# Kernel tuning notes

Hardware: AMD Instinct MI355X
Metric: run time of the kernel (lower is better)

The kernel has to match this reference:

```python
import jax, jax.numpy as jnp
import numpy as np

MEM_DIM = 4000
FEATURES = 2048
THRESHOLD = 1.0 / MEM_DIM
EPS = 1e-12
COS_EPS = 1e-8  # torch CosineSimilarity default eps


def setup_inputs() -> dict:
    key = jax.random.key(0)
    k1, k2 = jax.random.split(key)
    x = jax.random.normal(k1, (8192, FEATURES), dtype=jnp.float32)
    # kaiming_uniform_ with a=0: bound = sqrt(6 / fan_in), fan_in = FEATURES
    bound = float(np.sqrt(6.0 / FEATURES))
    memory = jax.random.uniform(k2, (MEM_DIM, FEATURES), dtype=jnp.float32,
                                minval=-bound, maxval=bound)
    return {"x": x, "memory": memory}


def reference(x, memory):
    # Cosine similarity via normalized matmul: [b, MEM_DIM]
    z_norm = jnp.linalg.norm(x, axis=1)              # [b]
    m_norm = jnp.linalg.norm(memory, axis=1)         # [M]
    logits = (x @ memory.T) / jnp.maximum(z_norm[:, None] * m_norm[None, :], COS_EPS)
    w = jax.nn.softmax(logits, axis=1)               # [b, M]
    # sparse shrinkage: relu(w - t) * w / (|w - t| + eps)
    d = w - THRESHOLD
    w = jnp.maximum(d, 0.0) * w / (jnp.abs(d) + EPS)
    # L1 normalize over memory dim (F.normalize p=1, eps=1e-12)
    w = w / jnp.maximum(jnp.sum(jnp.abs(w), axis=1, keepdims=True), EPS)
    return w @ memory                                # [b, features]
```

## Files before the change

kernel.cpp:

```cpp
#include <hip/hip_runtime.h>
#include <hip/hip_fp16.h>
#include <math.h>

#define FEATURES 2048
#define MROWS 4000
#define NPAD 4096
#define BROWS 8192

typedef unsigned short u16;
typedef unsigned int u32;

typedef __attribute__((ext_vector_type(8))) _Float16 f16x8;
typedef __attribute__((ext_vector_type(8))) short s16x8;
typedef __attribute__((ext_vector_type(4))) float f32x4;

__device__ __forceinline__ u16 f2h(float f) {
  union { _Float16 h; u16 u; } cv;
  cv.h = (_Float16)f;
  return cv.u;
}
__device__ __forceinline__ u16 f2bf(float f) {
  u32 u = __float_as_uint(f);
  u32 r = (u + 0x7FFFu + ((u >> 16) & 1u)) >> 16;
  return (u16)r;
}
__device__ __forceinline__ float bf2f(u16 h) {
  return __uint_as_float(((u32)h) << 16);
}

#define GLD16(g, l)                                                            \
  __builtin_amdgcn_global_load_lds(                                            \
      (const __attribute__((address_space(1))) u32*)(g),                       \
      (__attribute__((address_space(3))) u32*)(l), 16, 0, 0)

__global__ __launch_bounds__(256) void conv_split_bf16_kernel(
    const float* __restrict__ src, u16* __restrict__ hi, u16* __restrict__ lo,
    float* __restrict__ norms, int nrows) {
  __shared__ float red[4];
  const int row = blockIdx.x;
  const int tid = threadIdx.x;
  ushort4* hp = (ushort4*)(hi + (size_t)row * FEATURES);
  ushort4* lp = (ushort4*)(lo + (size_t)row * FEATURES);
  float ss = 0.f;
  if (row < nrows) {
    const float4* sp = (const float4*)(src + (size_t)row * FEATURES);
#pragma unroll
    for (int p = 0; p < 2; ++p) {
      const int idx = tid + p * 256;
      float4 f = sp[idx];
      ushort4 h, l;
      h.x = f2bf(f.x); l.x = f2bf(f.x - bf2f(h.x)); ss += f.x * f.x;
      h.y = f2bf(f.y); l.y = f2bf(f.y - bf2f(h.y)); ss += f.y * f.y;
      h.z = f2bf(f.z); l.z = f2bf(f.z - bf2f(h.z)); ss += f.z * f.z;
      h.w = f2bf(f.w); l.w = f2bf(f.w - bf2f(h.w)); ss += f.w * f.w;
      hp[idx] = h;
      lp[idx] = l;
    }
  } else {
    const ushort4 zz = {0, 0, 0, 0};
#pragma unroll
    for (int p = 0; p < 2; ++p) {
      hp[tid + p * 256] = zz;
      lp[tid + p * 256] = zz;
    }
  }
#pragma unroll
  for (int o = 32; o; o >>= 1) ss += __shfl_xor(ss, o);
  if ((tid & 63) == 0) red[tid >> 6] = ss;
  __syncthreads();
  if (tid == 0) {
    float tot = red[0] + red[1] + red[2] + red[3];
    norms[row] = (row < nrows) ? sqrtf(tot) : 1.0f;
  }
}

__global__ __launch_bounds__(256) void transpose_f16_kernel(
    const float* __restrict__ mem, u16* __restrict__ mt) {
  __shared__ float tile[64][65];
  const int tid = threadIdx.x;
  const int ti = blockIdx.x;
  const int tj = blockIdx.y;
  const int c = tid & 63;
  const int r0 = tid >> 6;
#pragma unroll
  for (int i = 0; i < 16; ++i) {
    const int r = i * 4 + r0;
    const int gr = ti * 64 + r;
    float v = 0.f;
    if (gr < MROWS) v = mem[(size_t)gr * FEATURES + tj * 64 + c];
    tile[r][c] = v;
  }
  __syncthreads();
#pragma unroll
  for (int i = 0; i < 16; ++i) {
    const int r = i * 4 + r0;
    mt[(size_t)(tj * 64 + r) * NPAD + ti * 64 + c] = f2h(tile[c][r]);
  }
}

__global__ __launch_bounds__(512, 2) void gemm1_kernel(
    const u16* __restrict__ Ah, const u16* __restrict__ Al,
    const u16* __restrict__ Bh, const u16* __restrict__ Bl,
    const float* __restrict__ zn, const float* __restrict__ mn,
    float* __restrict__ C) {
  __shared__ __align__(16) u16 sAh[2 * 8192];
  __shared__ __align__(16) u16 sAl[2 * 8192];
  __shared__ __align__(16) u16 sBh[2 * 8192];
  __shared__ __align__(16) u16 sBl[2 * 8192];
  const int tid = threadIdx.x;
  const int wid = tid >> 6;
  const int lane = tid & 63;
  const int brow = blockIdx.x * 256;
  const int bcol = blockIdx.y * 256;
  const int wr = wid >> 2;
  const int wc = wid & 3;
  const int fr = lane & 15, fq = lane >> 4;
  const int fqa = (fq ^ ((fr >> 1) & 3)) * 8;

  f32x4 acc[8][4];
#pragma unroll
  for (int m = 0; m < 8; ++m)
#pragma unroll
    for (int n = 0; n < 4; ++n) acc[m][n] = (f32x4){0.f, 0.f, 0.f, 0.f};

  const int r_st = tid >> 2;
  const int c_sw = (((tid & 3) ^ ((tid >> 3) & 3)) << 3);

#define STAGE1(cur, k0)                                                        \
  {                                                                            \
    _Pragma("unroll") for (int p = 0; p < 2; ++p) {                            \
      const int r = r_st + p * 128;                                            \
      const size_t offA = (size_t)(brow + r) * FEATURES + ((k0) + c_sw);       \
      const size_t offB = (size_t)(bcol + r) * FEATURES + ((k0) + c_sw);       \
      const int ldso = (cur) * 8192 + p * 4096 + wid * 512;                    \
      GLD16(Ah + offA, sAh + ldso);                                            \
      GLD16(Al + offA, sAl + ldso);                                            \
      GLD16(Bh + offB, sBh + ldso);                                            \
      GLD16(Bl + offB, sBl + ldso);                                            \
    }                                                                          \
  }

#define G1_COMPUTE(cur)                                                        \
  {                                                                            \
    const int bo = (cur) * 8192;                                               \
    s16x8 bh[4], bl[4];                                                        \
    _Pragma("unroll") for (int n = 0; n < 4; ++n) {                            \
      const int ro = bo + (wc * 64 + n * 16 + fr) * 32 + fqa;                  \
      bh[n] = *(const s16x8*)(sBh + ro);                                       \
      bl[n] = *(const s16x8*)(sBl + ro);                                       \
    }                                                                          \
    _Pragma("unroll") for (int m = 0; m < 8; ++m) {                            \
      const int ro = bo + (wr * 128 + m * 16 + fr) * 32 + fqa;                 \
      const s16x8 ah = *(const s16x8*)(sAh + ro);                              \
      const s16x8 al = *(const s16x8*)(sAl + ro);                              \
      _Pragma("unroll") for (int n = 0; n < 4; ++n) {                          \
        acc[m][n] = __builtin_amdgcn_mfma_f32_16x16x32_bf16(                   \
            ah, bh[n], acc[m][n], 0, 0, 0);                                    \
        acc[m][n] = __builtin_amdgcn_mfma_f32_16x16x32_bf16(                   \
            al, bh[n], acc[m][n], 0, 0, 0);                                    \
        acc[m][n] = __builtin_amdgcn_mfma_f32_16x16x32_bf16(                   \
            ah, bl[n], acc[m][n], 0, 0, 0);                                    \
      }                                                                        \
    }                                                                          \
  }

  STAGE1(0, 0);
  __syncthreads();
  for (int kt = 0; kt < 64; ++kt) {
    const int cur = kt & 1;
    if (kt < 63) STAGE1(cur ^ 1, (kt + 1) * 32);
    G1_COMPUTE(cur);
    __syncthreads();
  }
#undef STAGE1
#undef G1_COMPUTE

#pragma unroll
  for (int m = 0; m < 8; ++m) {
#pragma unroll
    for (int r = 0; r < 4; ++r) {
      const int row = brow + wr * 128 + m * 16 + fq * 4 + r;
      const float z = zn[row];
#pragma unroll
      for (int n = 0; n < 4; ++n) {
        const int col = bcol + wc * 64 + n * 16 + fr;
        const float denom = fmaxf(z * mn[col], 1e-8f);
        C[(size_t)row * NPAD + col] = acc[m][n][r] / denom;
      }
    }
  }
}

__global__ __launch_bounds__(256) void softmax_kernel(float* __restrict__ logits) {
  __shared__ float red[4];
  const int row = blockIdx.x;
  const int tid = threadIdx.x;
  const float* lp = logits + (size_t)row * NPAD;
  u16* W = (u16*)logits + (size_t)row * (2 * NPAD);
  float v[16];
  float lmax = -3.4e38f;
#pragma unroll
  for (int i = 0; i < 16; ++i) {
    const int c = tid + i * 256;
    v[i] = (c < MROWS) ? lp[c] : -3.4e38f;
    lmax = fmaxf(lmax, v[i]);
  }
#pragma unroll
  for (int o = 32; o; o >>= 1) lmax = fmaxf(lmax, __shfl_xor(lmax, o));
  if ((tid & 63) == 0) red[tid >> 6] = lmax;
  __syncthreads();
  lmax = fmaxf(fmaxf(red[0], red[1]), fmaxf(red[2], red[3]));

  float s = 0.f;
#pragma unroll
  for (int i = 0; i < 16; ++i) {
    const int c = tid + i * 256;
    if (c < MROWS) {
      v[i] = expf(v[i] - lmax);
      s += v[i];
    } else {
      v[i] = 0.f;
    }
  }
#pragma unroll
  for (int o = 32; o; o >>= 1) s += __shfl_xor(s, o);
  __syncthreads();
  if ((tid & 63) == 0) red[tid >> 6] = s;
  __syncthreads();
  const float Z = red[0] + red[1] + red[2] + red[3];

  const float THR = (float)(1.0 / 4000.0);
  float s2 = 0.f;
#pragma unroll
  for (int i = 0; i < 16; ++i) {
    float w = v[i] / Z;
    const float d = w - THR;
    w = fmaxf(d, 0.f) * w / (fabsf(d) + 1e-12f);
    v[i] = w;
    s2 += w;
  }
#pragma unroll
  for (int o = 32; o; o >>= 1) s2 += __shfl_xor(s2, o);
  __syncthreads();
  if ((tid & 63) == 0) red[tid >> 6] = s2;
  __syncthreads();
  const float S = fmaxf(red[0] + red[1] + red[2] + red[3], 1e-12f);

#pragma unroll
  for (int i = 0; i < 16; ++i) {
    const int c = tid + i * 256;
    W[c] = f2h(v[i] / S);
  }
}

__global__ __launch_bounds__(256) void gemm2_kernel(
    const u16* __restrict__ A, const u16* __restrict__ B,
    float* __restrict__ C) {
  __shared__ __align__(16) u16 sA[2 * 4096];
  __shared__ __align__(16) u16 sB[2 * 4096];
  const int tid = threadIdx.x;
  const int wid = tid >> 6;
  const int lane = tid & 63;
  const int brow = blockIdx.x * 128;
  const int bcol = blockIdx.y * 128;
  const int wr = wid >> 1, wc = wid & 1;
  const int fr = lane & 15, fq = lane >> 4;
  const int fqa = (fq ^ ((fr >> 1) & 3)) * 8;

  f32x4 acc[4][4];
#pragma unroll
  for (int m = 0; m < 4; ++m)
#pragma unroll
    for (int n = 0; n < 4; ++n) acc[m][n] = (f32x4){0.f, 0.f, 0.f, 0.f};

  const int r_st = tid >> 2;
  const int c_sw = (((tid & 3) ^ ((tid >> 3) & 3)) << 3);

#define STAGE2(cur, k0)                                                        \
  {                                                                            \
    _Pragma("unroll") for (int p = 0; p < 2; ++p) {                            \
      const int r = r_st + p * 64;                                             \
      const size_t offA = (size_t)(brow + r) * (2 * NPAD) + ((k0) + c_sw);     \
      const size_t offB = (size_t)(bcol + r) * NPAD + ((k0) + c_sw);           \
      const int ldso = (cur) * 4096 + p * 2048 + wid * 512;                    \
      GLD16(A + offA, sA + ldso);                                              \
      GLD16(B + offB, sB + ldso);                                              \
    }                                                                          \
  }

#define G2_COMPUTE(cur)                                                        \
  {                                                                            \
    const int bo = (cur) * 4096;                                               \
    f16x8 af[4], bf[4];                                                        \
    _Pragma("unroll") for (int m = 0; m < 4; ++m)                              \
      af[m] = *(const f16x8*)(sA + bo + (wr * 64 + m * 16 + fr) * 32 + fqa);   \
    _Pragma("unroll") for (int n = 0; n < 4; ++n)                              \
      bf[n] = *(const f16x8*)(sB + bo + (wc * 64 + n * 16 + fr) * 32 + fqa);   \
    _Pragma("unroll") for (int m = 0; m < 4; ++m)                              \
      _Pragma("unroll") for (int n = 0; n < 4; ++n)                            \
        acc[m][n] = __builtin_amdgcn_mfma_f32_16x16x32_f16(                    \
            af[m], bf[n], acc[m][n], 0, 0, 0);                                 \
  }

  STAGE2(0, 0);
  __syncthreads();
  for (int kt = 0; kt < 128; ++kt) {
    const int cur = kt & 1;
    if (kt < 127) STAGE2(cur ^ 1, (kt + 1) * 32);
    G2_COMPUTE(cur);
    __syncthreads();
  }
#undef STAGE2
#undef G2_COMPUTE

#pragma unroll
  for (int m = 0; m < 4; ++m) {
#pragma unroll
    for (int r = 0; r < 4; ++r) {
      const int row = brow + wr * 64 + m * 16 + fq * 4 + r;
#pragma unroll
      for (int n = 0; n < 4; ++n) {
        const int col = bcol + wc * 64 + n * 16 + fr;
        C[(size_t)row * FEATURES + col] = acc[m][n][r];
      }
    }
  }
}

extern "C" void kernel_launch(void* const* d_in, const int* in_sizes, int n_in,
                              void* d_out, int out_size, void* d_ws, size_t ws_size,
                              hipStream_t stream) {
  const float* x = (const float*)d_in[0];
  const float* mem = (const float*)d_in[1];
  float* out = (float*)d_out;
  char* ws = (char*)d_ws;

  size_t o = 0;
  u16* mh = (u16*)(ws + o); o += (size_t)NPAD * FEATURES * 2;
  u16* ml = (u16*)(ws + o); o += (size_t)NPAD * FEATURES * 2;
  u16* mt = (u16*)(ws + o); o += (size_t)FEATURES * NPAD * 2;
  float* zn = (float*)(ws + o); o += (size_t)BROWS * 4;
  float* mn = (float*)(ws + o); o += (size_t)NPAD * 4;
  const size_t base = o;

  int CH = BROWS;
  size_t need = 0;
  for (;; CH >>= 1) {
    need = base + (size_t)CH * FEATURES * 2 * 2 + (size_t)CH * NPAD * 4;
    if (need <= ws_size || CH == 256) break;
  }
  if (need > ws_size) return;
  u16* xh = (u16*)(ws + base);
  u16* xl = (u16*)(ws + base + (size_t)CH * FEATURES * 2);
  float* lg = (float*)(ws + base + (size_t)CH * FEATURES * 4);

  conv_split_bf16_kernel<<<NPAD, 256, 0, stream>>>(mem, mh, ml, mn, MROWS);
  transpose_f16_kernel<<<dim3(NPAD / 64, FEATURES / 64), 256, 0, stream>>>(mem, mt);

  for (int r0 = 0; r0 < BROWS; r0 += CH) {
    conv_split_bf16_kernel<<<CH, 256, 0, stream>>>(x + (size_t)r0 * FEATURES, xh, xl, zn, CH);
    gemm1_kernel<<<dim3(CH / 256, NPAD / 256), 512, 0, stream>>>(xh, xl, mh, ml, zn, mn, lg);
    softmax_kernel<<<CH, 256, 0, stream>>>(lg);
    gemm2_kernel<<<dim3(CH / 128, FEATURES / 128), 256, 0, stream>>>(
        (const u16*)lg, mt, out + (size_t)r0 * FEATURES);
  }
}
```

Before: 590.7 us.

## Enlarge gemm2 tiles to 256x256 with 512 threads and add XCD-aware block swizzle

gemm2 goes from 128x128 tiles with 4 waves to 256x256 tiles with 8 waves, each wave computing 128x64, so every LDS and global load feeds more MFMA work. Both GEMMs also remap block indices so that neighbouring tiles land on the same XCD, improving L2 reuse of shared operand rows. The trade-off is higher register and LDS use per block, which may lower occupancy, and fewer blocks for the gemm2 grid.

```diff
diff --git a/kernel.cpp b/kernel.cpp
--- a/kernel.cpp
+++ b/kernel.cpp
@@ -32,6 +32,15 @@
   __builtin_amdgcn_global_load_lds(                                            \
       (const __attribute__((address_space(1))) u32*)(g),                       \
       (__attribute__((address_space(3))) u32*)(l), 16, 0, 0)
+
+__device__ __forceinline__ void xcd_swz(int& bx, int& by) {
+  const int nbx = gridDim.x;
+  const int nwg = nbx * gridDim.y;
+  int flat = bx + nbx * by;
+  flat = (flat & 7) * (nwg >> 3) + (flat >> 3);
+  bx = flat % nbx;
+  by = flat / nbx;
+}
 
 __global__ __launch_bounds__(256) void conv_split_bf16_kernel(
     const float* __restrict__ src, u16* __restrict__ hi, u16* __restrict__ lo,
@@ -110,8 +119,10 @@
   const int tid = threadIdx.x;
   const int wid = tid >> 6;
   const int lane = tid & 63;
-  const int brow = blockIdx.x * 256;
-  const int bcol = blockIdx.y * 256;
+  int bix = blockIdx.x, biy = blockIdx.y;
+  xcd_swz(bix, biy);
+  const int brow = bix * 256;
+  const int bcol = biy * 256;
   const int wr = wid >> 2;
   const int wc = wid & 3;
   const int fr = lane & 15, fq = lane >> 4;
@@ -253,23 +264,25 @@
   }
 }
 
-__global__ __launch_bounds__(256) void gemm2_kernel(
+__global__ __launch_bounds__(512, 2) void gemm2_kernel(
     const u16* __restrict__ A, const u16* __restrict__ B,
     float* __restrict__ C) {
-  __shared__ __align__(16) u16 sA[2 * 4096];
-  __shared__ __align__(16) u16 sB[2 * 4096];
+  __shared__ __align__(16) u16 sA[2 * 8192];
+  __shared__ __align__(16) u16 sB[2 * 8192];
   const int tid = threadIdx.x;
   const int wid = tid >> 6;
   const int lane = tid & 63;
-  const int brow = blockIdx.x * 128;
-  const int bcol = blockIdx.y * 128;
-  const int wr = wid >> 1, wc = wid & 1;
+  int bix = blockIdx.x, biy = blockIdx.y;
+  xcd_swz(bix, biy);
+  const int brow = bix * 256;
+  const int bcol = biy * 256;
+  const int wr = wid >> 2, wc = wid & 3;
   const int fr = lane & 15, fq = lane >> 4;
   const int fqa = (fq ^ ((fr >> 1) & 3)) * 8;
 
-  f32x4 acc[4][4];
-#pragma unroll
-  for (int m = 0; m < 4; ++m)
+  f32x4 acc[8][4];
+#pragma unroll
+  for (int m = 0; m < 8; ++m)
 #pragma unroll
     for (int n = 0; n < 4; ++n) acc[m][n] = (f32x4){0.f, 0.f, 0.f, 0.f};
 
@@ -279,10 +292,10 @@
 #define STAGE2(cur, k0)                                                        \
   {                                                                            \
     _Pragma("unroll") for (int p = 0; p < 2; ++p) {                            \
-      const int r = r_st + p * 64;                                             \
+      const int r = r_st + p * 128;                                            \
       const size_t offA = (size_t)(brow + r) * (2 * NPAD) + ((k0) + c_sw);     \
       const size_t offB = (size_t)(bcol + r) * NPAD + ((k0) + c_sw);           \
-      const int ldso = (cur) * 4096 + p * 2048 + wid * 512;                    \
+      const int ldso = (cur) * 8192 + p * 4096 + wid * 512;                    \
       GLD16(A + offA, sA + ldso);                                              \
       GLD16(B + offB, sB + ldso);                                              \
     }                                                                          \
@@ -290,16 +303,17 @@
 
 #define G2_COMPUTE(cur)                                                        \
   {                                                                            \
-    const int bo = (cur) * 4096;                                               \
-    f16x8 af[4], bf[4];                                                        \
-    _Pragma("unroll") for (int m = 0; m < 4; ++m)                              \
-      af[m] = *(const f16x8*)(sA + bo + (wr * 64 + m * 16 + fr) * 32 + fqa);   \
+    const int bo = (cur) * 8192;                                               \
+    f16x8 bf[4];                                                               \
     _Pragma("unroll") for (int n = 0; n < 4; ++n)                              \
       bf[n] = *(const f16x8*)(sB + bo + (wc * 64 + n * 16 + fr) * 32 + fqa);   \
-    _Pragma("unroll") for (int m = 0; m < 4; ++m)                              \
+    _Pragma("unroll") for (int m = 0; m < 8; ++m) {                            \
+      const f16x8 af =                                                         \
+          *(const f16x8*)(sA + bo + (wr * 128 + m * 16 + fr) * 32 + fqa);      \
       _Pragma("unroll") for (int n = 0; n < 4; ++n)                            \
         acc[m][n] = __builtin_amdgcn_mfma_f32_16x16x32_f16(                    \
-            af[m], bf[n], acc[m][n], 0, 0, 0);                                 \
+            af, bf[n], acc[m][n], 0, 0, 0);                                    \
+    }                                                                          \
   }
 
   STAGE2(0, 0);
@@ -314,10 +328,10 @@
 #undef G2_COMPUTE
 
 #pragma unroll
-  for (int m = 0; m < 4; ++m) {
+  for (int m = 0; m < 8; ++m) {
 #pragma unroll
     for (int r = 0; r < 4; ++r) {
-      const int row = brow + wr * 64 + m * 16 + fq * 4 + r;
+      const int row = brow + wr * 128 + m * 16 + fq * 4 + r;
 #pragma unroll
       for (int n = 0; n < 4; ++n) {
         const int col = bcol + wc * 64 + n * 16 + fr;
@@ -361,7 +375,7 @@
     conv_split_bf16_kernel<<<CH, 256, 0, stream>>>(x + (size_t)r0 * FEATURES, xh, xl, zn, CH);
     gemm1_kernel<<<dim3(CH / 256, NPAD / 256), 512, 0, stream>>>(xh, xl, mh, ml, zn, mn, lg);
     softmax_kernel<<<CH, 256, 0, stream>>>(lg);
-    gemm2_kernel<<<dim3(CH / 128, FEATURES / 128), 256, 0, stream>>>(
+    gemm2_kernel<<<dim3(CH / 256, FEATURES / 256), 512, 0, stream>>>(
         (const u16*)lg, mt, out + (size_t)r0 * FEATURES);
   }
 }
```

Result: slower. 762.5 us (+29.1%).
